# Optimization experiments

Hardware: AMD Instinct MI355X
Metric: run time of the kernel (lower is better)

The kernel has to match this reference:

```python
import jax, jax.numpy as jnp
import numpy as np

NODE_FEATURES = 256
HIDDEN = 32
N_NODES = 100000
N_EDGES = 3200000


def _glorot(key, shape):
    fan_in, fan_out = shape[-2], shape[-1]
    lim = (6.0 / (fan_in + fan_out)) ** 0.5
    return jax.random.uniform(key, shape, jnp.float32, -lim, lim)


def setup_inputs() -> dict:
    key = jax.random.key(0)
    ks = jax.random.split(key, 12)
    in_cat = NODE_FEATURES + HIDDEN  # DConv input is cat([X, H])
    x = jax.random.normal(ks[0], (N_NODES, NODE_FEATURES), jnp.float32)
    edge_index = jax.random.randint(ks[1], (2, N_EDGES), 0, N_NODES, jnp.int64)
    return {
        "x": x,
        "edge_index": edge_index,
        # DConv weights have shape (2, K=1, in, out); squeeze K -> (2, in, out)
        "w_z": _glorot(ks[2], (2, in_cat, HIDDEN)),
        "b_z": jnp.zeros((HIDDEN,), jnp.float32),
        "w_r": _glorot(ks[3], (2, in_cat, HIDDEN)),
        "b_r": jnp.zeros((HIDDEN,), jnp.float32),
        "w_h": _glorot(ks[4], (2, in_cat, HIDDEN)),
        "b_h": jnp.zeros((HIDDEN,), jnp.float32),
        # fc head, stored as [in, out]
        "fc1_w": _glorot(ks[5], (HIDDEN, HIDDEN)),
        "fc1_b": jnp.zeros((HIDDEN,), jnp.float32),
        "fc2_w": _glorot(ks[6], (HIDDEN, 1)),
        "fc2_b": jnp.zeros((1,), jnp.float32),
    }


def _dconv_k1(inp, w, b):
    # K=1 DConv: only the k=0 Chebyshev term for both diffusion directions,
    # i.e. no propagation over edges. H = X @ W_out + X @ W_in + bias.
    return inp @ (w[0] + w[1]) + b


def reference(x, edge_index, w_z, b_z, w_r, b_r, w_h, b_h, fc1_w, fc1_b, fc2_w, fc2_b):
    n = x.shape[0]
    h0 = jnp.zeros((n, HIDDEN), x.dtype)  # DCRNN called with H=None -> zeros
    xh0 = jnp.concatenate([x, h0], axis=1)  # [N, F+H]
    z = jax.nn.sigmoid(_dconv_k1(xh0, w_z, b_z))  # update gate
    r = jax.nn.sigmoid(_dconv_k1(xh0, w_r, b_r))  # reset gate
    xrh = jnp.concatenate([x, r * h0], axis=1)
    h_tilde = jnp.tanh(_dconv_k1(xrh, w_h, b_h))
    h = z * h0 + (1.0 - z) * h_tilde  # [N, 32]
    # fc head: Linear-ReLU-Dropout(eval=identity)-Linear-Sigmoid
    hidden = jax.nn.relu(h @ fc1_w + fc1_b)
    out = jax.nn.sigmoid(hidden @ fc2_w + fc2_b)  # [N, 1]
    return out
```

## Files before the change

kernel.cpp:

```cpp
#include <hip/hip_runtime.h>
#include <hip/hip_bf16.h>


#define NF    256
#define TILE  32
#define NPB   64
#define NTHR  256
#define CSTR  68
#define HKT   8

typedef __attribute__((ext_vector_type(8)))  short  short8;
typedef __attribute__((ext_vector_type(16))) float  floatx16;
typedef __attribute__((ext_vector_type(4)))  float  f32x4;

__device__ __forceinline__ unsigned f2bf(float f) {
    __hip_bfloat16 h = __float2bfloat16(f);
    return (unsigned)*(unsigned short*)&h;
}
__device__ __forceinline__ float fast_sigmoid(float v) {
    return 1.0f / (1.0f + __expf(-v));
}
__device__ __forceinline__ float fast_tanh(float v) {
    return 1.0f - 2.0f / (1.0f + __expf(2.0f * v));
}

__global__ void prep_W(const float* __restrict__ wz,
                       const float* __restrict__ wh,
                       unsigned short* __restrict__ Wf)
{
    int idx = blockIdx.x * blockDim.x + threadIdx.x;
    if (idx >= NF * 64) return;
    int j    = idx & 7;
    int lane = (idx >> 3) & 63;
    int nt   = (idx >> 9) & 1;
    int kt   = idx >> 10;
    int k = kt * 16 + (lane >> 5) * 8 + j;
    int o = nt * 32 + (lane & 31);
    const int PLANE = 288 * 32;
    float v;
    if (o < 32) v = wz[k * 32 + o]        + wz[PLANE + k * 32 + o];
    else        v = wh[k * 32 + (o - 32)] + wh[PLANE + k * 32 + (o - 32)];
    Wf[idx] = (unsigned short)f2bf(v);
}

__global__ void __launch_bounds__(NTHR, 5)
rgcn_main(const float* __restrict__ x,
          const unsigned short* __restrict__ Wf,
          const float* __restrict__ bz,
          const float* __restrict__ bh,
          const float* __restrict__ fc1w,
          const float* __restrict__ fc1b,
          const float* __restrict__ fc2w,
          const float* __restrict__ fc2b,
          float* __restrict__ out,
          int n_nodes)
{
    __shared__ __align__(16) float Xc[NPB * CSTR];

    const int tid   = threadIdx.x;
    const int lane  = tid & 63;
    const int wave  = tid >> 6;
    const int tile  = wave & 1;
    const int khalf = wave >> 1;
    const int node0 = blockIdx.x * NPB;

    const int nc = lane & 31;
    int gn = node0 + tile * TILE + nc;
    if (gn >= n_nodes) gn = n_nodes - 1;
    const float* xr = x + (size_t)gn * NF + khalf * 128 + (lane >> 5) * 8;

    floatx16 acc0 = {};
    floatx16 acc1 = {};

#pragma unroll
    for (int kt = 0; kt < HKT; ++kt) {
        f32x4 v0 = __builtin_nontemporal_load((const f32x4*)(xr + kt * 16));
        f32x4 v1 = __builtin_nontemporal_load((const f32x4*)(xr + kt * 16 + 4));
        int g = khalf * HKT + kt;
        uint4 b0u = ((const uint4*)Wf)[(size_t)(g * 2 + 0) * 64 + lane];
        uint4 b1u = ((const uint4*)Wf)[(size_t)(g * 2 + 1) * 64 + lane];
        union { short8 s; unsigned u[4]; } a, b0, b1;
        a.u[0] = f2bf(v0.x) | (f2bf(v0.y) << 16);
        a.u[1] = f2bf(v0.z) | (f2bf(v0.w) << 16);
        a.u[2] = f2bf(v1.x) | (f2bf(v1.y) << 16);
        a.u[3] = f2bf(v1.z) | (f2bf(v1.w) << 16);
        b0.u[0] = b0u.x; b0.u[1] = b0u.y; b0.u[2] = b0u.z; b0.u[3] = b0u.w;
        b1.u[0] = b1u.x; b1.u[1] = b1u.y; b1.u[2] = b1u.z; b1.u[3] = b1u.w;
        acc0 = __builtin_amdgcn_mfma_f32_32x32x16_bf16(a.s, b0.s, acc0, 0, 0, 0);
        acc1 = __builtin_amdgcn_mfma_f32_32x32x16_bf16(a.s, b1.s, acc1, 0, 0, 0);
    }

    if (khalf == 1) {
#pragma unroll
        for (int r = 0; r < 16; ++r) {
            int row = (r & 3) + 8 * (r >> 2) + 4 * (lane >> 5);
            int base = (tile * TILE + row) * CSTR;
            Xc[base + nc]      = acc0[r];
            Xc[base + 32 + nc] = acc1[r];
        }
    }
    __syncthreads();

    if (khalf == 0) {
        const float bzn = bz[nc];
        const float bhn = bh[nc];
#pragma unroll
        for (int r = 0; r < 16; ++r) {
            int row = (r & 3) + 8 * (r >> 2) + 4 * (lane >> 5);
            int base = (tile * TILE + row) * CSTR;
            float s0 = acc0[r] + Xc[base + nc];
            float s1 = acc1[r] + Xc[base + 32 + nc];
            float z = fast_sigmoid(s0 + bzn);
            float t = fast_tanh   (s1 + bhn);
            acc0[r] = (1.0f - z) * t;
        }
    }
    __syncthreads();
    if (khalf == 0) {
#pragma unroll
        for (int r = 0; r < 16; ++r) {
            int row = (r & 3) + 8 * (r >> 2) + 4 * (lane >> 5);
            Xc[(tile * TILE + row) * CSTR + nc] = acc0[r];
        }
    }
    __syncthreads();

    if (khalf == 0) {
        const int nl   = nc;
        const int half = lane >> 5;
        const float* hp = Xc + (tile * TILE + nl) * CSTR;
        float h[32];
#pragma unroll
        for (int q = 0; q < 8; ++q) {
            float4 v = *(const float4*)(hp + q * 4);
            h[q * 4 + 0] = v.x; h[q * 4 + 1] = v.y;
            h[q * 4 + 2] = v.z; h[q * 4 + 3] = v.w;
        }
        float part = 0.0f;
        for (int jj = 0; jj < 16; ++jj) {
            int j = (half << 4) + jj;
            float s = fc1b[j];
#pragma unroll
            for (int o = 0; o < 32; ++o)
                s = fmaf(h[o], fc1w[o * 32 + j], s);
            part = fmaf(fmaxf(s, 0.0f), fc2w[j], part);
        }
        part += __shfl_xor(part, 32);
        if (half == 0) {
            int g = node0 + tile * TILE + nl;
            if (g < n_nodes)
                out[g] = fast_sigmoid(part + fc2b[0]);
        }
    }
}

extern "C" void kernel_launch(void* const* d_in, const int* in_sizes, int n_in,
                              void* d_out, int out_size, void* d_ws, size_t ws_size,
                              hipStream_t stream) {
    const float* x    = (const float*)d_in[0];
    const float* wz   = (const float*)d_in[2];
    const float* bz   = (const float*)d_in[3];
    const float* wh   = (const float*)d_in[6];
    const float* bh   = (const float*)d_in[7];
    const float* fc1w = (const float*)d_in[8];
    const float* fc1b = (const float*)d_in[9];
    const float* fc2w = (const float*)d_in[10];
    const float* fc2b = (const float*)d_in[11];
    float* out = (float*)d_out;
    unsigned short* Wf = (unsigned short*)d_ws;

    const int n = in_sizes[0] / NF;

    prep_W<<<(NF * 64 + 255) / 256, 256, 0, stream>>>(wz, wh, Wf);
    rgcn_main<<<(n + NPB - 1) / NPB, NTHR, 0, stream>>>(
        x, Wf, bz, bh, fc1w, fc1b, fc2w, fc2b, out, n);
}
```

Before: 208.4 us.

## Split K across four waves per 32-node tile and drop barriers in epilogue

Each block now handles 32 nodes instead of 64, with its four waves splitting the 256-wide reduction into quarters instead of two tiles times two halves. Three waves write partial sums to shared memory and wave 0 reduces them. Wave 0 then runs the gating and FC head on its own, using an explicit LDS waitcnt in place of two block barriers. This doubles the block count and shortens each wave's serial MFMA chain, which should expose more memory parallelism. The cost is more LDS traffic for partials and a longer single-wave epilogue.

```diff
diff --git a/kernel.cpp b/kernel.cpp
--- a/kernel.cpp
+++ b/kernel.cpp
@@ -4,10 +4,9 @@
 
 #define NF    256
 #define TILE  32
-#define NPB   64
 #define NTHR  256
+#define QKT   4
 #define CSTR  68
-#define HKT   8
 
 typedef __attribute__((ext_vector_type(8)))  short  short8;
 typedef __attribute__((ext_vector_type(16))) float  floatx16;
@@ -55,28 +54,26 @@
           float* __restrict__ out,
           int n_nodes)
 {
-    __shared__ __align__(16) float Xc[NPB * CSTR];
+    __shared__ __align__(16) float Pc[3 * TILE * CSTR];
 
     const int tid   = threadIdx.x;
     const int lane  = tid & 63;
-    const int wave  = tid >> 6;
-    const int tile  = wave & 1;
-    const int khalf = wave >> 1;
-    const int node0 = blockIdx.x * NPB;
+    const int q     = tid >> 6;
+    const int node0 = blockIdx.x * TILE;
 
     const int nc = lane & 31;
-    int gn = node0 + tile * TILE + nc;
+    int gn = node0 + nc;
     if (gn >= n_nodes) gn = n_nodes - 1;
-    const float* xr = x + (size_t)gn * NF + khalf * 128 + (lane >> 5) * 8;
+    const float* xr = x + (size_t)gn * NF + q * 64 + (lane >> 5) * 8;
 
     floatx16 acc0 = {};
     floatx16 acc1 = {};
 
 #pragma unroll
-    for (int kt = 0; kt < HKT; ++kt) {
+    for (int kt = 0; kt < QKT; ++kt) {
         f32x4 v0 = __builtin_nontemporal_load((const f32x4*)(xr + kt * 16));
         f32x4 v1 = __builtin_nontemporal_load((const f32x4*)(xr + kt * 16 + 4));
-        int g = khalf * HKT + kt;
+        int g = q * QKT + kt;
         uint4 b0u = ((const uint4*)Wf)[(size_t)(g * 2 + 0) * 64 + lane];
         uint4 b1u = ((const uint4*)Wf)[(size_t)(g * 2 + 1) * 64 + lane];
         union { short8 s; unsigned u[4]; } a, b0, b1;
@@ -90,51 +87,50 @@
         acc1 = __builtin_amdgcn_mfma_f32_32x32x16_bf16(a.s, b1.s, acc1, 0, 0, 0);
     }
 
-    if (khalf == 1) {
+    if (q > 0) {
+        float* P = Pc + (q - 1) * TILE * CSTR;
 #pragma unroll
         for (int r = 0; r < 16; ++r) {
             int row = (r & 3) + 8 * (r >> 2) + 4 * (lane >> 5);
-            int base = (tile * TILE + row) * CSTR;
-            Xc[base + nc]      = acc0[r];
-            Xc[base + 32 + nc] = acc1[r];
+            P[row * CSTR + nc]      = acc0[r];
+            P[row * CSTR + 32 + nc] = acc1[r];
         }
     }
     __syncthreads();
 
-    if (khalf == 0) {
+    if (q == 0) {
         const float bzn = bz[nc];
         const float bhn = bh[nc];
+        float* P0 = Pc;
+        float* P1 = Pc + TILE * CSTR;
+        float* P2 = Pc + 2 * TILE * CSTR;
 #pragma unroll
         for (int r = 0; r < 16; ++r) {
-            int row = (r & 3) + 8 * (r >> 2) + 4 * (lane >> 5);
-            int base = (tile * TILE + row) * CSTR;
-            float s0 = acc0[r] + Xc[base + nc];
-            float s1 = acc1[r] + Xc[base + 32 + nc];
+            int row  = (r & 3) + 8 * (r >> 2) + 4 * (lane >> 5);
+            int base = row * CSTR;
+            float s0 = acc0[r] + P0[base + nc] + P1[base + nc] + P2[base + nc];
+            float s1 = acc1[r] + P0[base + 32 + nc] + P1[base + 32 + nc]
+                               + P2[base + 32 + nc];
             float z = fast_sigmoid(s0 + bzn);
             float t = fast_tanh   (s1 + bhn);
             acc0[r] = (1.0f - z) * t;
         }
-    }
-    __syncthreads();
-    if (khalf == 0) {
 #pragma unroll
         for (int r = 0; r < 16; ++r) {
             int row = (r & 3) + 8 * (r >> 2) + 4 * (lane >> 5);
-            Xc[(tile * TILE + row) * CSTR + nc] = acc0[r];
+            P0[row * CSTR + nc] = acc0[r];
         }
-    }
-    __syncthreads();
+        asm volatile("s_waitcnt lgkmcnt(0)" ::: "memory");
 
-    if (khalf == 0) {
         const int nl   = nc;
         const int half = lane >> 5;
-        const float* hp = Xc + (tile * TILE + nl) * CSTR;
+        const float* hp = P0 + nl * CSTR;
         float h[32];
 #pragma unroll
-        for (int q = 0; q < 8; ++q) {
-            float4 v = *(const float4*)(hp + q * 4);
-            h[q * 4 + 0] = v.x; h[q * 4 + 1] = v.y;
-            h[q * 4 + 2] = v.z; h[q * 4 + 3] = v.w;
+        for (int m = 0; m < 8; ++m) {
+            float4 v = *(const float4*)(hp + m * 4);
+            h[m * 4 + 0] = v.x; h[m * 4 + 1] = v.y;
+            h[m * 4 + 2] = v.z; h[m * 4 + 3] = v.w;
         }
         float part = 0.0f;
         for (int jj = 0; jj < 16; ++jj) {
@@ -147,7 +143,7 @@
         }
         part += __shfl_xor(part, 32);
         if (half == 0) {
-            int g = node0 + tile * TILE + nl;
+            int g = node0 + nl;
             if (g < n_nodes)
                 out[g] = fast_sigmoid(part + fc2b[0]);
         }
@@ -172,6 +168,6 @@
     const int n = in_sizes[0] / NF;
 
     prep_W<<<(NF * 64 + 255) / 256, 256, 0, stream>>>(wz, wh, Wf);
-    rgcn_main<<<(n + NPB - 1) / NPB, NTHR, 0, stream>>>(
+    rgcn_main<<<(n + TILE - 1) / TILE, NTHR, 0, stream>>>(
         x, Wf, bz, bh, fc1w, fc1b, fc2w, fc2b, out, n);
 }
```

Result: no change. 206.5 us (-0.9%).
